# Performance work log

Hardware: AMD Instinct MI355X
Metric: run time of the kernel (lower is better)

## Reference

```python
import math
import jax, jax.numpy as jnp
import numpy as np

B, N, M, C, H = 64, 64, 64, 512, 8
HD = C // H
FREQ = 256  # frequency_embedding_size
MAX_PERIOD = 10000.0


def setup_inputs() -> dict:
    key = jax.random.key(0)
    ks = jax.random.split(key, 10)
    s = 1.0 / math.sqrt(C)
    sf = 1.0 / math.sqrt(FREQ)
    return {
        "query": jax.random.normal(ks[0], (B, N, C), jnp.float32),
        "query_pos": jax.random.uniform(ks[1], (1, N, M), jnp.float32),
        # projection weights stored as [in, out]
        "Wq": jax.random.normal(ks[2], (C, C), jnp.float32) * s,
        "bq": jnp.zeros((C,), jnp.float32),
        "Wk": jax.random.normal(ks[3], (C, C), jnp.float32) * s,  # no bias
        "Wv": jax.random.normal(ks[4], (C, C), jnp.float32) * s,
        "bv": jnp.zeros((C,), jnp.float32),
        "Wo": jax.random.normal(ks[5], (C, C), jnp.float32) * s,
        "bo": jnp.zeros((C,), jnp.float32),
        # ScalarEmbedder MLP: Linear(FREQ->C), SiLU, Linear(C->C)
        "W1": jax.random.normal(ks[6], (FREQ, C), jnp.float32) * sf,
        "b1": jnp.zeros((C,), jnp.float32),
        "W2": jax.random.normal(ks[7], (C, C), jnp.float32) * s,
        "b2": jnp.zeros((C,), jnp.float32),
    }


def _freqs():
    half = FREQ // 2
    return jnp.exp(-math.log(MAX_PERIOD) * jnp.arange(half, dtype=jnp.float32) / half)


def reference(query, query_pos, Wq, bq, Wk, Wv, bv, Wo, bo, W1, b1, W2, b2):
    Bq, Nq, Cq = query.shape
    Mk = query_pos.shape[-1]
    # --- ScalarEmbedder on flattened pairwise positions: [N*M] -> [N*M, C]
    t = query_pos.reshape(-1)                       # [Bp*N*M], Bp = 1
    tf = t[:, None] * _freqs()[None, :]             # [N*M, FREQ/2]
    emb = jnp.concatenate([jnp.cos(tf), jnp.sin(tf)], axis=-1)  # [N*M, FREQ]
    pe = jax.nn.silu(emb @ W1 + b1) @ W2 + b2        # [N*M, C]
    pe = pe.reshape(Nq, Mk, H, HD).transpose(2, 0, 1, 3)  # [H, N, M, hd] (tiled over B via broadcast)

    q = (query @ Wq + bq).reshape(Bq, Nq, H, HD)     # bnhd
    k = (query @ Wk).reshape(Bq, Mk, H, HD)          # bmhd (key = query)
    v = (query @ Wv + bv).reshape(Bq, Mk, H, HD)

    scale = HD ** -0.5
    # attn[b,h,n,m] = sum_d q[b,n,h,d] * pe[h,n,m,d] * k[b,m,h,d]
    scores = jnp.einsum("bnhd,hnmd,bmhd->bhnm", q, pe, k) * scale
    attn = jax.nn.softmax(scores, axis=-1)
    x = jnp.einsum("bhnm,bmhd->bnhd", attn, v).reshape(Bq, Nq, Cq)
    return x @ Wo + bo + query  # identity = query
```

## Files before the change

### kernel.cpp

```cpp
#include <hip/hip_runtime.h>
#include <hip/hip_bf16.h>
#include <math.h>

typedef short short8 __attribute__((ext_vector_type(8)));
typedef float floatx4 __attribute__((ext_vector_type(4)));

__device__ __forceinline__ ushort f2bf(float f) {
    __hip_bfloat16 h = __float2bfloat16(f);
    return *reinterpret_cast<ushort*>(&h);
}
__device__ __forceinline__ void bf8_to_f32(uint4 u, float* f) {
    f[0] = __uint_as_float(u.x << 16); f[1] = __uint_as_float(u.x & 0xffff0000u);
    f[2] = __uint_as_float(u.y << 16); f[3] = __uint_as_float(u.y & 0xffff0000u);
    f[4] = __uint_as_float(u.z << 16); f[5] = __uint_as_float(u.z & 0xffff0000u);
    f[6] = __uint_as_float(u.w << 16); f[7] = __uint_as_float(u.w & 0xffff0000u);
}

#define GLDS16(g, l) __builtin_amdgcn_global_load_lds( \
    (const __attribute__((address_space(1))) void*)(g), \
    (__attribute__((address_space(3))) void*)(l), 16, 0, 0)

__global__ __launch_bounds__(256) void prep_kernel(
        const float* __restrict__ W1, const float* __restrict__ W2,
        const float* __restrict__ Wq, const float* __restrict__ Wk,
        const float* __restrict__ Wv, const float* __restrict__ Wo,
        const float* __restrict__ bq, const float* __restrict__ bv,
        const float* __restrict__ query, const float* __restrict__ qpos,
        ushort* __restrict__ W1t, ushort* __restrict__ W2t,
        ushort* __restrict__ Wqkvt, ushort* __restrict__ Wot,
        ushort* __restrict__ queryB, ushort* __restrict__ embB,
        float* __restrict__ biasC) {
    const int z = blockIdx.z;
    const int tx = threadIdx.x, ty = threadIdx.y;
    const int tid = ty * 32 + tx;
    if (z < 6) {
        const float* src; ushort* dst; int R;
        switch (z) {
            case 0:  src = W1; dst = W1t;              R = 256; break;
            case 1:  src = W2; dst = W2t;              R = 512; break;
            case 2:  src = Wq; dst = Wqkvt;            R = 512; break;
            case 3:  src = Wk; dst = Wqkvt + 512*512;  R = 512; break;
            case 4:  src = Wv; dst = Wqkvt + 1024*512; R = 512; break;
            default: src = Wo; dst = Wot;              R = 512; break;
        }
        const int r0 = blockIdx.y * 32, c0 = blockIdx.x * 32;
        if (r0 >= R) return;
        __shared__ float t[32][33];
        for (int i = ty; i < 32; i += 8) t[i][tx] = src[(size_t)(r0 + i) * 512 + c0 + tx];
        __syncthreads();
        for (int i = ty; i < 32; i += 8) dst[(size_t)(c0 + i) * R + r0 + tx] = f2bf(t[tx][i]);
    } else if (z == 6) {
        const int bid = blockIdx.y * 16 + blockIdx.x;
#pragma unroll
        for (int i = 0; i < 8; ++i) {
            size_t idx4 = (size_t)bid * 2048 + i * 256 + tid;
            float4 v = *(const float4*)(query + idx4 * 4);
            ushort4 o; o.x = f2bf(v.x); o.y = f2bf(v.y); o.z = f2bf(v.z); o.w = f2bf(v.w);
            *(ushort4*)(queryB + idx4 * 4) = o;
        }
        if (bid == 0) {
            for (int i = tid; i < 1536; i += 256)
                biasC[i] = (i < 512) ? bq[i] : ((i < 1024) ? 0.0f : bv[i - 1024]);
        }
    } else {
        const int bid = blockIdx.y * 16 + blockIdx.x;
        const int gt = bid * 256 + tid;
        const int e0 = gt * 16;
        const int r = e0 >> 8, j0 = e0 & 255;
        const float t = qpos[r];
        ushort o[16];
#pragma unroll
        for (int u = 0; u < 16; ++u) {
            int j = j0 + u, i = j & 127;
            float freq = __expf(-9.210340371976184f * (float)i * (1.0f / 128.0f));
            float a = t * freq;
            o[u] = f2bf((j < 128) ? __cosf(a) : __sinf(a));
        }
        *(uint4*)(embB + e0)     = *(uint4*)&o[0];
        *(uint4*)(embB + e0 + 8) = *(uint4*)&o[8];
    }
}

struct GArgs {
    const ushort* A; const ushort* Bt; const float* bias; const float* resid;
    void* C; int N, K, act, outf32, ntn;
};

template<int BM, int BN>
__global__ __launch_bounds__(256) void gemm_multi(GArgs g0, GArgs g1, int split) {
    constexpr int MR = BM / 32;
    constexpr int NR = BN / 32;
    __shared__ ushort As[2][BM * 32];
    __shared__ ushort Bs[2][BN * 32];

    const bool sel = ((int)blockIdx.x >= split);
    const GArgs g = sel ? g1 : g0;
    const int bid = sel ? ((int)blockIdx.x - split) : (int)blockIdx.x;
    const int tm = bid / g.ntn, tn = bid % g.ntn;
    const int row0 = tm * BM, col0 = tn * BN;
    const int K = g.K, N = g.N;

    const int tid = threadIdx.x;
    const int l = tid & 63, w = tid >> 6;
    const int wr = w >> 1, wc = w & 1;
    const int l15 = l & 15, quad = l >> 4;

    const int srow = tid >> 2;
    const int skoff = (tid & 3) * 8;
    const ushort* gA = g.A  + (size_t)(row0 + srow) * K + skoff;
    const ushort* gB = g.Bt + (size_t)(col0 + srow) * K + skoff;

    auto stage = [&](int s, int k0) {
#pragma unroll
        for (int i = 0; i < BM / 64; ++i)
            GLDS16(gA + (size_t)(i * 64) * K + k0, &As[s][(i * 256 + tid) * 8]);
#pragma unroll
        for (int i = 0; i < BN / 64; ++i)
            GLDS16(gB + (size_t)(i * 64) * K + k0, &Bs[s][(i * 256 + tid) * 8]);
    };

    floatx4 acc[MR][NR] = {};

    const int nk = K >> 5;
    stage(0, 0);
    int cur = 0;
    for (int t = 0; t < nk; ++t) {
        __syncthreads();
        if (t + 1 < nk) stage(cur ^ 1, (t + 1) * 32);
        short8 af[MR], bf[NR];
#pragma unroll
        for (int m = 0; m < MR; ++m)
            af[m] = *(const short8*)&As[cur][(wr * (BM / 2) + m * 16 + l15) * 32 + quad * 8];
#pragma unroll
        for (int n = 0; n < NR; ++n)
            bf[n] = *(const short8*)&Bs[cur][(wc * (BN / 2) + n * 16 + l15) * 32 + quad * 8];
#pragma unroll
        for (int m = 0; m < MR; ++m)
#pragma unroll
            for (int n = 0; n < NR; ++n)
                acc[m][n] = __builtin_amdgcn_mfma_f32_16x16x32_bf16(af[m], bf[n], acc[m][n], 0, 0, 0);
        cur ^= 1;
    }

#pragma unroll
    for (int m = 0; m < MR; ++m)
#pragma unroll
        for (int n = 0; n < NR; ++n) {
            int col = col0 + wc * (BN / 2) + n * 16 + l15;
            float bvv = g.bias ? g.bias[col] : 0.0f;
#pragma unroll
            for (int r = 0; r < 4; ++r) {
                int row = row0 + wr * (BM / 2) + m * 16 + quad * 4 + r;
                float val = acc[m][n][r] + bvv;
                if (g.act) val = val / (1.0f + __expf(-val));
                if (g.outf32) {
                    float rv = g.resid ? g.resid[(size_t)row * N + col] : 0.0f;
                    ((float*)g.C)[(size_t)row * N + col] = val + rv;
                } else {
                    ((ushort*)g.C)[(size_t)row * N + col] = f2bf(val);
                }
            }
        }
}

__global__ __launch_bounds__(256) void attn_bf16(
        const ushort* __restrict__ qkv, const ushort* __restrict__ peB,
        ushort* __restrict__ xB) {
    constexpr int LP = 68;
    constexpr int PP = 66;
    const int h = blockIdx.x, b = blockIdx.y, nh = blockIdx.z;
    const int tid = threadIdx.x;
    const int w = tid >> 6, l = tid & 63;
    const int lo = l & 7, hi = l >> 3;

    __shared__ float ks[64 * LP];
    __shared__ float vs[64 * LP];
    __shared__ ushort ps[32 * PP];

#pragma unroll
    for (int p = 0; p < 2; ++p) {
        int cid = p * 256 + tid;
        int row = cid >> 3, ch = cid & 7;
        const ushort* base = qkv + (size_t)(b * 64 + row) * 1536 + h * 64 + ch * 8;
        uint4 ku = *(const uint4*)(base + 512);
        uint4 vu = *(const uint4*)(base + 1024);
        float kf[8], vf[8];
        bf8_to_f32(ku, kf); bf8_to_f32(vu, vf);
#pragma unroll
        for (int j = 0; j < 8; ++j) {
            ks[row * LP + ch * 8 + j] = kf[j];
            vs[row * LP + ch * 8 + j] = vf[j];
        }
    }
    __syncthreads();

    for (int i = 0; i < 8; ++i) {
        int nl = w + 4 * i;
        int n = nh * 32 + nl;

        uint4 qu = *(const uint4*)(qkv + (size_t)(b * 64 + n) * 1536 + h * 64 + lo * 8);
        float qf[8]; bf8_to_f32(qu, qf);

        uint4 pu[8];
#pragma unroll
        for (int mg = 0; mg < 8; ++mg)
            pu[mg] = *(const uint4*)(peB + (size_t)(n * 64 + mg * 8 + hi) * 512 + h * 64 + lo * 8);

        float sreg[8];
#pragma unroll
        for (int mg = 0; mg < 8; ++mg) {
            int m = mg * 8 + hi;
            float pf[8]; bf8_to_f32(pu[mg], pf);
            float kf[8];
            *(float4*)&kf[0] = *(const float4*)&ks[m * LP + lo * 8];
            *(float4*)&kf[4] = *(const float4*)&ks[m * LP + lo * 8 + 4];
            float p = 0.0f;
#pragma unroll
            for (int j = 0; j < 8; ++j) p = fmaf(qf[j] * kf[j], pf[j], p);
            p += __shfl_xor(p, 1);
            p += __shfl_xor(p, 2);
            p += __shfl_xor(p, 4);
            sreg[mg] = p * 0.125f;
        }

        float mx = sreg[0];
#pragma unroll
        for (int mg = 1; mg < 8; ++mg) mx = fmaxf(mx, sreg[mg]);
        mx = fmaxf(mx, __shfl_xor(mx, 8));
        mx = fmaxf(mx, __shfl_xor(mx, 16));
        mx = fmaxf(mx, __shfl_xor(mx, 32));
        float sum = 0.0f;
#pragma unroll
        for (int mg = 0; mg < 8; ++mg) { sreg[mg] = __expf(sreg[mg] - mx); sum += sreg[mg]; }
        sum += __shfl_xor(sum, 8);
        sum += __shfl_xor(sum, 16);
        sum += __shfl_xor(sum, 32);
        float rs = 1.0f / sum;

        float pv = sreg[0];
#pragma unroll
        for (int mg = 1; mg < 8; ++mg) if (lo == mg) pv = sreg[mg];
        ps[nl * PP + 8 * lo + hi] = f2bf(pv * rs);
    }
    __syncthreads();

    {
        const int n8 = tid >> 3, dch = tid & 7;
        float acc[8] = {};
#pragma unroll 4
        for (int m = 0; m < 64; ++m) {
            float at = __uint_as_float(((uint)ps[n8 * PP + m]) << 16);
            float vf[8];
            *(float4*)&vf[0] = *(const float4*)&vs[m * LP + dch * 8];
            *(float4*)&vf[4] = *(const float4*)&vs[m * LP + dch * 8 + 4];
#pragma unroll
            for (int j = 0; j < 8; ++j) acc[j] = fmaf(at, vf[j], acc[j]);
        }
        int n = nh * 32 + n8;
        uint4 o;
        o.x = f2bf(acc[0]) | ((uint)f2bf(acc[1]) << 16);
        o.y = f2bf(acc[2]) | ((uint)f2bf(acc[3]) << 16);
        o.z = f2bf(acc[4]) | ((uint)f2bf(acc[5]) << 16);
        o.w = f2bf(acc[6]) | ((uint)f2bf(acc[7]) << 16);
        *(uint4*)(xB + (size_t)(b * 64 + n) * 512 + h * 64 + dch * 8) = o;
    }
}

extern "C" void kernel_launch(void* const* d_in, const int* in_sizes, int n_in,
                              void* d_out, int out_size, void* d_ws, size_t ws_size,
                              hipStream_t stream) {
    const float* query = (const float*)d_in[0];
    const float* qpos  = (const float*)d_in[1];
    const float* Wq    = (const float*)d_in[2];
    const float* bq    = (const float*)d_in[3];
    const float* Wk    = (const float*)d_in[4];
    const float* Wv    = (const float*)d_in[5];
    const float* bv    = (const float*)d_in[6];
    const float* Wo    = (const float*)d_in[7];
    const float* bo    = (const float*)d_in[8];
    const float* W1    = (const float*)d_in[9];
    const float* b1    = (const float*)d_in[10];
    const float* W2    = (const float*)d_in[11];
    const float* b2    = (const float*)d_in[12];
    float* out = (float*)d_out;
    char* ws = (char*)d_ws;

    ushort* W1t    = (ushort*)(ws + 0);
    ushort* W2t    = (ushort*)(ws + 262144);
    ushort* Wqkvt  = (ushort*)(ws + 786432);
    ushort* Wot    = (ushort*)(ws + 2359296);
    float*  biasC  = (float*) (ws + 2883584);
    ushort* embB   = (ushort*)(ws + 3145728);
    ushort* queryB = (ushort*)(ws + 5242880);
    ushort* hiddenB= (ushort*)(ws + 9437184);
    ushort* peB    = (ushort*)(ws + 13631488);
    ushort* qkvB   = (ushort*)(ws + 17825792);
    ushort* xB     = (ushort*)(ws + 30408704);

    prep_kernel<<<dim3(16, 16, 8), dim3(32, 8), 0, stream>>>(
        W1, W2, Wq, Wk, Wv, Wo, bq, bv, query, qpos,
        W1t, W2t, Wqkvt, Wot, queryB, embB, biasC);

    GArgs a_g1 { embB,    W1t,   b1,    nullptr, hiddenB, 512,  256, 1, 0, 8  };
    GArgs a_g2 { hiddenB, W2t,   b2,    nullptr, peB,     512,  512, 0, 0, 8  };
    GArgs a_qkv{ queryB,  Wqkvt, biasC, nullptr, qkvB,    1536, 512, 0, 0, 24 };
    GArgs a_out{ xB,      Wot,   bo,    query,   out,     512,  512, 0, 1, 8  };

    gemm_multi<64, 64><<<512, 256, 0, stream>>>(a_g1, a_g1, 1 << 30);
    gemm_multi<64, 64><<<2048, 256, 0, stream>>>(a_g2, a_qkv, 512);

    attn_bf16<<<dim3(8, 64, 2), 256, 0, stream>>>(qkvB, peB, xB);

    gemm_multi<64, 64><<<512, 256, 0, stream>>>(a_out, a_out, 1 << 30);
}
```

Baseline: 157.5 us.

## Use MFMA for attention-times-V and keep K in registers as bf16

Rewrites the attention kernel's PV product to use bf16 16x16x32 MFMA instructions, with V stored transposed as bf16 in shared memory instead of fp32. K rows are loaded directly into registers per lane instead of staged in shared memory, and the first barrier is removed. This cuts LDS footprint and scalar FMA work, at the cost of more register pressure and scalar 2-byte output stores.

```diff
diff --git a/kernel.cpp b/kernel.cpp
--- a/kernel.cpp
+++ b/kernel.cpp
@@ -166,33 +166,34 @@
 __global__ __launch_bounds__(256) void attn_bf16(
         const ushort* __restrict__ qkv, const ushort* __restrict__ peB,
         ushort* __restrict__ xB) {
-    constexpr int LP = 68;
-    constexpr int PP = 66;
+    constexpr int PT = 72;
     const int h = blockIdx.x, b = blockIdx.y, nh = blockIdx.z;
     const int tid = threadIdx.x;
     const int w = tid >> 6, l = tid & 63;
     const int lo = l & 7, hi = l >> 3;
-
-    __shared__ float ks[64 * LP];
-    __shared__ float vs[64 * LP];
-    __shared__ ushort ps[32 * PP];
-
-#pragma unroll
-    for (int p = 0; p < 2; ++p) {
-        int cid = p * 256 + tid;
-        int row = cid >> 3, ch = cid & 7;
-        const ushort* base = qkv + (size_t)(b * 64 + row) * 1536 + h * 64 + ch * 8;
-        uint4 ku = *(const uint4*)(base + 512);
-        uint4 vu = *(const uint4*)(base + 1024);
-        float kf[8], vf[8];
-        bf8_to_f32(ku, kf); bf8_to_f32(vu, vf);
+    const int l15 = l & 15, quad = l >> 4;
+
+    __shared__ ushort vsT[64 * PT];
+    __shared__ ushort ps[32 * PT];
+
+    {
+        const int rp = tid >> 3, ch = tid & 7;
+        const ushort* vb = qkv + (size_t)(b * 64 + 2 * rp) * 1536 + h * 64 + 1024 + ch * 8;
+        uint4 v0 = *(const uint4*)vb;
+        uint4 v1 = *(const uint4*)(vb + 1536);
+        const ushort* a0 = (const ushort*)&v0;
+        const ushort* a1 = (const ushort*)&v1;
 #pragma unroll
         for (int j = 0; j < 8; ++j) {
-            ks[row * LP + ch * 8 + j] = kf[j];
-            vs[row * LP + ch * 8 + j] = vf[j];
-        }
-    }
-    __syncthreads();
+            uint pk = (uint)a0[j] | ((uint)a1[j] << 16);
+            *(uint*)&vsT[(ch * 8 + j) * PT + 2 * rp] = pk;
+        }
+    }
+
+    short8 ku[8];
+#pragma unroll
+    for (int mg = 0; mg < 8; ++mg)
+        ku[mg] = *(const short8*)(qkv + (size_t)(b * 64 + mg * 8 + hi) * 1536 + h * 64 + 512 + lo * 8);
 
     for (int i = 0; i < 8; ++i) {
         int nl = w + 4 * i;
@@ -209,14 +210,14 @@
         float sreg[8];
 #pragma unroll
         for (int mg = 0; mg < 8; ++mg) {
-            int m = mg * 8 + hi;
             float pf[8]; bf8_to_f32(pu[mg], pf);
-            float kf[8];
-            *(float4*)&kf[0] = *(const float4*)&ks[m * LP + lo * 8];
-            *(float4*)&kf[4] = *(const float4*)&ks[m * LP + lo * 8 + 4];
+            const ushort* kk = (const ushort*)&ku[mg];
             float p = 0.0f;
 #pragma unroll
-            for (int j = 0; j < 8; ++j) p = fmaf(qf[j] * kf[j], pf[j], p);
+            for (int j = 0; j < 8; ++j) {
+                float kfj = __uint_as_float(((uint)kk[j]) << 16);
+                p = fmaf(qf[j] * kfj, pf[j], p);
+            }
             p += __shfl_xor(p, 1);
             p += __shfl_xor(p, 2);
             p += __shfl_xor(p, 4);
@@ -240,29 +241,30 @@
         float pv = sreg[0];
 #pragma unroll
         for (int mg = 1; mg < 8; ++mg) if (lo == mg) pv = sreg[mg];
-        ps[nl * PP + 8 * lo + hi] = f2bf(pv * rs);
+        ps[nl * PT + 8 * lo + hi] = f2bf(pv * rs);
     }
     __syncthreads();
 
     {
-        const int n8 = tid >> 3, dch = tid & 7;
-        float acc[8] = {};
-#pragma unroll 4
-        for (int m = 0; m < 64; ++m) {
-            float at = __uint_as_float(((uint)ps[n8 * PP + m]) << 16);
-            float vf[8];
-            *(float4*)&vf[0] = *(const float4*)&vs[m * LP + dch * 8];
-            *(float4*)&vf[4] = *(const float4*)&vs[m * LP + dch * 8 + 4];
-#pragma unroll
-            for (int j = 0; j < 8; ++j) acc[j] = fmaf(at, vf[j], acc[j]);
-        }
-        int n = nh * 32 + n8;
-        uint4 o;
-        o.x = f2bf(acc[0]) | ((uint)f2bf(acc[1]) << 16);
-        o.y = f2bf(acc[2]) | ((uint)f2bf(acc[3]) << 16);
-        o.z = f2bf(acc[4]) | ((uint)f2bf(acc[5]) << 16);
-        o.w = f2bf(acc[6]) | ((uint)f2bf(acc[7]) << 16);
-        *(uint4*)(xB + (size_t)(b * 64 + n) * 512 + h * 64 + dch * 8) = o;
+        const int ntile = w & 1;
+        const int dt0 = (w >> 1) << 1;
+        floatx4 o0 = {0.f, 0.f, 0.f, 0.f};
+        floatx4 o1 = {0.f, 0.f, 0.f, 0.f};
+#pragma unroll
+        for (int ks = 0; ks < 2; ++ks) {
+            short8 a  = *(const short8*)&ps[(ntile * 16 + l15) * PT + ks * 32 + quad * 8];
+            short8 b0 = *(const short8*)&vsT[((dt0    ) * 16 + l15) * PT + ks * 32 + quad * 8];
+            short8 b1 = *(const short8*)&vsT[((dt0 + 1) * 16 + l15) * PT + ks * 32 + quad * 8];
+            o0 = __builtin_amdgcn_mfma_f32_16x16x32_bf16(a, b0, o0, 0, 0, 0);
+            o1 = __builtin_amdgcn_mfma_f32_16x16x32_bf16(a, b1, o1, 0, 0, 0);
+        }
+        const int nbase = nh * 32 + ntile * 16 + quad * 4;
+#pragma unroll
+        for (int r = 0; r < 4; ++r) {
+            size_t rowoff = (size_t)(b * 64 + nbase + r) * 512 + h * 64;
+            xB[rowoff + (dt0    ) * 16 + l15] = f2bf(o0[r]);
+            xB[rowoff + (dt0 + 1) * 16 + l15] = f2bf(o1[r]);
+        }
     }
 }
 
```

After: 158.0 us. About the same (+0.3%).
